# Kernel tuning notes

Measured on AMD Instinct MI355X. Metric: run time of the kernel, lower is better.

## Reference

```python
import jax, jax.numpy as jnp
import numpy as np

PLACEHOLDER = -1
TINY = np.float32(np.finfo(np.float32).tiny)

B, S, V = 128, 8, 32000  # batch, max_spec_len, vocab


def setup_inputs() -> dict:
    key = jax.random.key(0)
    ks = jax.random.split(key, 8)
    # probability tables from softmaxed logits (faithful: rows sum to 1)
    draft_probs = jax.nn.softmax(2.0 * jax.random.normal(ks[0], (B, S, V), dtype=jnp.float32), axis=-1)
    target_probs = jax.nn.softmax(2.0 * jax.random.normal(ks[1], (B, S + 1, V), dtype=jnp.float32), axis=-1)
    draft_token_ids = jax.random.randint(ks[2], (B, S), 0, V, dtype=jnp.int64)
    # variable number of draft tokens per sequence; tail padded with PLACEHOLDER
    lens = jax.random.randint(ks[3], (B,), 1, S + 1)
    draft_token_ids = jnp.where(jnp.arange(S)[None, :] < lens[:, None], draft_token_ids, PLACEHOLDER)
    bonus_token_ids = jax.random.randint(ks[4], (B,), 0, V, dtype=jnp.int64)
    uniform_probs = jax.random.uniform(ks[5], (B, S), dtype=jnp.float32, minval=1e-6, maxval=1.0)
    exp_q = jax.random.exponential(ks[6], (B, V), dtype=jnp.float32)  # q.exponential_()
    is_greedy = jax.random.bernoulli(ks[7], 0.3, (B,))  # temperature == -1 per sequence
    return {
        "draft_token_ids": draft_token_ids,
        "draft_probs": draft_probs,
        "target_probs": target_probs,
        "bonus_token_ids": bonus_token_ids,
        "uniform_probs": uniform_probs,
        "exp_q": exp_q,
        "is_greedy": is_greedy,
    }


def reference(draft_token_ids, draft_probs, target_probs, bonus_token_ids,
              uniform_probs, exp_q, is_greedy):
    b, s = draft_token_ids.shape
    valid = draft_token_ids != PLACEHOLDER                      # [B,S]
    safe_tok = jnp.where(valid, draft_token_ids, 0)

    # gather p_target(tok), p_draft(tok) at each speculative position
    tp = jnp.take_along_axis(target_probs[:, :s], safe_tok[..., None], axis=2)[..., 0]
    dp = jnp.take_along_axis(draft_probs, safe_tok[..., None], axis=2)[..., 0]
    random_accept = (tp / dp) >= uniform_probs                  # [B,S]

    target_argmax = jnp.argmax(target_probs, axis=-1)           # [B,S+1]
    greedy_accept = draft_token_ids == target_argmax[:, :s]

    accept = jnp.where(is_greedy[:, None], greedy_accept, random_accept)

    # recovered token on rejection: argmax of normalized clamp(target - draft) / Exp noise
    adjusted = jnp.clip(target_probs[:, :s] - draft_probs, TINY, None)
    adjusted = adjusted / jnp.sum(adjusted, axis=-1, keepdims=True)
    recovered = jnp.argmax(adjusted / exp_q[:, None, :], axis=-1)  # [B,S]
    replacement = jnp.where(is_greedy[:, None], target_argmax[:, :s], recovered)

    # sequential early-exit scan, vectorized: position p emits iff all earlier
    # positions were valid & accepted and p itself is valid
    step = (valid & accept).astype(jnp.int32)
    alive_prefix = jnp.concatenate(
        [jnp.ones((b, 1), jnp.int32), jnp.cumprod(step, axis=1)[:, :-1]], axis=1).astype(bool)
    emit = valid & alive_prefix                                 # [B,S]

    tokens = jnp.where(accept, draft_token_ids, replacement)
    out = jnp.full((b, s + 1), PLACEHOLDER, dtype=jnp.int64)
    out = out.at[:, :s].set(jnp.where(emit, tokens, PLACEHOLDER))

    num_generated = jnp.sum(emit, axis=1)                       # [B]
    rejected = jnp.any(emit & ~accept, axis=1)                  # [B]
    bonus_val = jnp.where(rejected, PLACEHOLDER, bonus_token_ids)
    out = out.at[jnp.arange(b), num_generated].set(bonus_val)
    return out
```

## Files before the change

### kernel.cpp

```cpp
#include <hip/hip_runtime.h>

#define PLACEHOLDER (-1)
#define TINY_F 1.17549435e-38f
#define MAXS 32
#define SPLIT_G 8
#define SPLIT_R 16

__device__ __forceinline__ void amax_combine(float& bv, int& bi, float v, int i) {
    if (v > bv || (v == bv && i < bi)) { bv = v; bi = i; }
}

__device__ __forceinline__ unsigned long long pack_vi(float v, int i) {
    return ((unsigned long long)__float_as_uint(v) << 32) |
           (unsigned long long)(0xFFFFFFFFu - (unsigned)i);
}

__device__ __forceinline__ int unpack_idx(unsigned long long p) {
    return (int)(0xFFFFFFFFu - (unsigned)(p & 0xFFFFFFFFull));
}

__device__ __forceinline__ void block_argmax(float& bv, int& bi) {
    for (int off = 32; off > 0; off >>= 1) {
        float ov = __shfl_down(bv, off, 64);
        int   oi = __shfl_down(bi, off, 64);
        amax_combine(bv, bi, ov, oi);
    }
    __shared__ float sv[8];
    __shared__ int   si[8];
    int lane = threadIdx.x & 63;
    int w    = threadIdx.x >> 6;
    if (lane == 0) { sv[w] = bv; si[w] = bi; }
    __syncthreads();
    if (threadIdx.x == 0) {
        int nw = (blockDim.x + 63) >> 6;
        for (int k = 1; k < nw; ++k) amax_combine(bv, bi, sv[k], si[k]);
    }
}

__device__ __forceinline__ void wave_argmax_bcast(float& bv, int& bi) {
    for (int off = 32; off > 0; off >>= 1) {
        float ov = __shfl_down(bv, off, 64);
        int   oi = __shfl_down(bi, off, 64);
        amax_combine(bv, bi, ov, oi);
    }
    bv = __shfl(bv, 0, 64);
    bi = __shfl(bi, 0, 64);
}

__global__ void k_main(const float* __restrict__ target_probs,
                       const float* __restrict__ draft_probs,
                       const float* __restrict__ exp_q,
                       const int* __restrict__ draft_ids,
                       const float* __restrict__ uniform,
                       const int* __restrict__ bonus,
                       const int* __restrict__ is_greedy,
                       unsigned long long* __restrict__ ws_g,
                       unsigned long long* __restrict__ ws_r,
                       int* __restrict__ ws_fr,
                       int* __restrict__ out,
                       int B, int S, int V) {
    int total_g = B * SPLIT_G;

    if ((int)blockIdx.x < total_g) {
        int b = blockIdx.x / SPLIT_G;
        int split = blockIdx.x - b * SPLIT_G;
        if (!is_greedy[b]) return;
        if (draft_ids[b * S] == PLACEHOLDER) return;

        int chunk = ((V + SPLIT_G - 1) / SPLIT_G + 3) & ~3;
        int begin = split * chunk;
        int end = begin + chunk; if (end > V) end = V;
        if (begin >= end) return;

        const float* row = target_probs + (size_t)b * (S + 1) * V;
        float bv = 0.0f; int bi = 0x7fffffff;
        int vend = begin + ((end - begin) & ~3);
        const float4* r4 = (const float4*)row;
        for (int j = (begin >> 2) + threadIdx.x; j < (vend >> 2); j += blockDim.x) {
            float4 f = r4[j];
            int base = j << 2;
            amax_combine(bv, bi, f.x, base);
            amax_combine(bv, bi, f.y, base + 1);
            amax_combine(bv, bi, f.z, base + 2);
            amax_combine(bv, bi, f.w, base + 3);
        }
        for (int j = vend + threadIdx.x; j < end; j += blockDim.x)
            amax_combine(bv, bi, row[j], j);
        block_argmax(bv, bi);
        if (threadIdx.x == 0) ws_g[(size_t)b * SPLIT_G + split] = pack_vi(bv, bi);
    } else {
        int t = blockIdx.x - total_g;
        int split = t % SPLIT_R;
        int b = t / SPLIT_R;
        if (is_greedy[b]) return;

        int chunk = ((V + SPLIT_R - 1) / SPLIT_R + 3) & ~3;
        int begin = split * chunk;
        int end = begin + chunk; if (end > V) end = V;
        bool has_work = begin < end;

        const float* erow = exp_q + (size_t)b * V;
        int nj = has_work ? (((end - begin) & ~3) >> 2) : 0;
        const float4* e4 = (const float4*)(erow + begin);
        int tid = threadIdx.x;
        float4 ea = make_float4(0.f, 0.f, 0.f, 0.f), eb = ea;
        if (tid < nj) ea = e4[tid];
        if (tid + (int)blockDim.x < nj) eb = e4[tid + blockDim.x];

        __shared__ int s_tok[MAXS];
        __shared__ unsigned char s_acc[MAXS];
        __shared__ int s_fr;
        if (tid < S) {
            int tok = draft_ids[b * S + tid];
            s_tok[tid] = tok;
            bool acc = false;
            if (tok != PLACEHOLDER) {
                float tp = target_probs[(size_t)b * (S + 1) * V + (size_t)tid * V + tok];
                float dp = draft_probs[(size_t)b * S * V + (size_t)tid * V + tok];
                acc = (tp / dp) >= uniform[b * S + tid];
            }
            s_acc[tid] = acc ? 1 : 0;
        }
        __syncthreads();
        if (tid == 0) {
            int fr = -1;
            for (int q = 0; q < S; ++q) {
                if (s_tok[q] == PLACEHOLDER) break;
                if (!s_acc[q]) { fr = q; break; }
            }
            s_fr = fr;
        }
        __syncthreads();
        int fr = s_fr;

        if (split == 0 && tid == 0) {
            ws_fr[b] = fr;
            int ob = b * (S + 1);
            if (fr < 0) {
                int ng = 0;
                for (int p = 0; p < S; ++p) {
                    if (s_tok[p] == PLACEHOLDER) break;
                    out[ob + p] = s_tok[p];
                    ++ng;
                }
                for (int q = ng; q <= S; ++q) out[ob + q] = PLACEHOLDER;
                out[ob + ng] = bonus[b];
            } else {
                for (int p = 0; p < fr; ++p) out[ob + p] = s_tok[p];
                for (int q = fr; q <= S; ++q) out[ob + q] = PLACEHOLDER;
            }
        }
        if (fr < 0 || !has_work) return;

        const float* trow = target_probs + (size_t)b * (S + 1) * V + (size_t)fr * V;
        const float* drow = draft_probs + (size_t)b * S * V + (size_t)fr * V;
        const float4* t4 = (const float4*)(trow + begin);
        const float4* d4 = (const float4*)(drow + begin);
        float bv = 0.0f; int bi = 0x7fffffff;
        if (tid < nj) {
            float4 tt = t4[tid], dd = d4[tid];
            int base = begin + (tid << 2);
            amax_combine(bv, bi, fmaxf(tt.x - dd.x, TINY_F) / ea.x, base);
            amax_combine(bv, bi, fmaxf(tt.y - dd.y, TINY_F) / ea.y, base + 1);
            amax_combine(bv, bi, fmaxf(tt.z - dd.z, TINY_F) / ea.z, base + 2);
            amax_combine(bv, bi, fmaxf(tt.w - dd.w, TINY_F) / ea.w, base + 3);
        }
        if (tid + (int)blockDim.x < nj) {
            int j = tid + blockDim.x;
            float4 tt = t4[j], dd = d4[j];
            int base = begin + (j << 2);
            amax_combine(bv, bi, fmaxf(tt.x - dd.x, TINY_F) / eb.x, base);
            amax_combine(bv, bi, fmaxf(tt.y - dd.y, TINY_F) / eb.y, base + 1);
            amax_combine(bv, bi, fmaxf(tt.z - dd.z, TINY_F) / eb.z, base + 2);
            amax_combine(bv, bi, fmaxf(tt.w - dd.w, TINY_F) / eb.w, base + 3);
        }
        for (int j = tid + 2 * blockDim.x; j < nj; j += blockDim.x) {
            float4 tt = t4[j], dd = d4[j], ee = e4[j];
            int base = begin + (j << 2);
            amax_combine(bv, bi, fmaxf(tt.x - dd.x, TINY_F) / ee.x, base);
            amax_combine(bv, bi, fmaxf(tt.y - dd.y, TINY_F) / ee.y, base + 1);
            amax_combine(bv, bi, fmaxf(tt.z - dd.z, TINY_F) / ee.z, base + 2);
            amax_combine(bv, bi, fmaxf(tt.w - dd.w, TINY_F) / ee.w, base + 3);
        }
        for (int j = begin + (nj << 2) + tid; j < end; j += blockDim.x)
            amax_combine(bv, bi, fmaxf(trow[j] - drow[j], TINY_F) / erow[j], j);
        block_argmax(bv, bi);
        if (tid == 0) ws_r[(size_t)b * SPLIT_R + split] = pack_vi(bv, bi);
    }
}

__global__ void k_final(const int* __restrict__ draft_ids,
                        const float* __restrict__ target_probs,
                        const int* __restrict__ bonus,
                        const int* __restrict__ is_greedy,
                        const unsigned long long* __restrict__ ws_g,
                        const unsigned long long* __restrict__ ws_r,
                        const int* __restrict__ ws_fr,
                        int* __restrict__ out,
                        int B, int S, int V) {
    int b = blockIdx.x;
    int lane = threadIdx.x;
    int ob = b * (S + 1);

    if (is_greedy[b]) {
        unsigned long long gm = 0ull;
        {
            int chunk = ((V + SPLIT_G - 1) / SPLIT_G + 3) & ~3;
            if (lane < SPLIT_G && lane * chunk < V)
                gm = ws_g[(size_t)b * SPLIT_G + lane];
        }
        for (int off = SPLIT_G / 2; off > 0; off >>= 1) {
            unsigned long long o = __shfl_down(gm, off, 64);
            if (o > gm) gm = o;
        }
        gm = __shfl(gm, 0, 64);
        int am0 = unpack_idx(gm);

        int p = 0, ng = 0;
        bool rej = false;
        while (p < S) {
            int tok = draft_ids[b * S + p];
            if (tok == PLACEHOLDER) break;
            int am;
            if (p == 0) {
                am = am0;
            } else {
                const float* row = target_probs + (size_t)b * (S + 1) * V + (size_t)p * V;
                float bv = 0.0f; int bi = 0x7fffffff;
                int nv4 = V >> 2;
                const float4* r4 = (const float4*)row;
                for (int j = lane; j < nv4; j += 64) {
                    float4 f = r4[j];
                    int base = j << 2;
                    amax_combine(bv, bi, f.x, base);
                    amax_combine(bv, bi, f.y, base + 1);
                    amax_combine(bv, bi, f.z, base + 2);
                    amax_combine(bv, bi, f.w, base + 3);
                }
                for (int j = (nv4 << 2) + lane; j < V; j += 64)
                    amax_combine(bv, bi, row[j], j);
                wave_argmax_bcast(bv, bi);
                am = bi;
            }
            bool acc = (tok == am);
            if (lane == 0) out[ob + p] = acc ? tok : am;
            ++ng;
            if (!acc) { rej = true; break; }
            ++p;
        }
        if (lane == 0) {
            for (int q = ng; q <= S; ++q) out[ob + q] = PLACEHOLDER;
            if (!rej) out[ob + ng] = bonus[b];
        }
    } else {
        int fr = ws_fr[b];
        if (fr < 0) return;
        unsigned long long rm = 0ull;
        {
            int chunk = ((V + SPLIT_R - 1) / SPLIT_R + 3) & ~3;
            if (lane < SPLIT_R && lane * chunk < V)
                rm = ws_r[(size_t)b * SPLIT_R + lane];
        }
        for (int off = SPLIT_R / 2; off > 0; off >>= 1) {
            unsigned long long o = __shfl_down(rm, off, 64);
            if (o > rm) rm = o;
        }
        if (lane == 0) out[ob + fr] = unpack_idx(rm);
    }
}

extern "C" void kernel_launch(void* const* d_in, const int* in_sizes, int n_in,
                              void* d_out, int out_size, void* d_ws, size_t ws_size,
                              hipStream_t stream) {
    const int*   draft_ids    = (const int*)d_in[0];
    const float* draft_probs  = (const float*)d_in[1];
    const float* target_probs = (const float*)d_in[2];
    const int*   bonus        = (const int*)d_in[3];
    const float* uniform      = (const float*)d_in[4];
    const float* exp_q        = (const float*)d_in[5];
    const int*   is_greedy    = (const int*)d_in[6];

    int B = in_sizes[6];
    int S = in_sizes[4] / B;
    int V = in_sizes[5] / B;

    unsigned long long* ws_g = (unsigned long long*)d_ws;
    unsigned long long* ws_r = ws_g + (size_t)B * SPLIT_G;
    int* ws_fr = (int*)(ws_r + (size_t)B * SPLIT_R);
    int* out = (int*)d_out;

    int grid = B * SPLIT_G + B * SPLIT_R;
    k_main<<<grid, 256, 0, stream>>>(target_probs, draft_probs, exp_q, draft_ids,
                                     uniform, bonus, is_greedy,
                                     ws_g, ws_r, ws_fr, out, B, S, V);
    k_final<<<B, 64, 0, stream>>>(draft_ids, target_probs, bonus, is_greedy,
                                  ws_g, ws_r, ws_fr, out, B, S, V);
}
```

Baseline: 15.21 us.

## Double vocab splits, reorder block roles, and early-exit greedy rejection at position zero

Doubles the number of vocabulary splits for both the greedy argmax and the recovered-token argmax, so more blocks share each row. The rejection-sampling blocks now come first in the grid, with the greedy blocks after them. Greedy blocks pre-fill the output row with placeholders, which lets the final kernel return immediately when the first draft token misses the target argmax. That early exit skips the sequential per-position argmax scan in the common rejection case. The trade-off is more blocks and more partial results to combine, plus output writes spread across two kernels.

```diff
diff --git a/kernel.cpp b/kernel.cpp
--- a/kernel.cpp
+++ b/kernel.cpp
@@ -3,8 +3,8 @@
 #define PLACEHOLDER (-1)
 #define TINY_F 1.17549435e-38f
 #define MAXS 32
-#define SPLIT_G 8
-#define SPLIT_R 16
+#define SPLIT_G 16
+#define SPLIT_R 32
 
 __device__ __forceinline__ void amax_combine(float& bv, int& bi, float v, int i) {
     if (v > bv || (v == bv && i < bi)) { bv = v; bi = i; }
@@ -59,39 +59,12 @@
                        int* __restrict__ ws_fr,
                        int* __restrict__ out,
                        int B, int S, int V) {
-    int total_g = B * SPLIT_G;
-
-    if ((int)blockIdx.x < total_g) {
-        int b = blockIdx.x / SPLIT_G;
-        int split = blockIdx.x - b * SPLIT_G;
-        if (!is_greedy[b]) return;
-        if (draft_ids[b * S] == PLACEHOLDER) return;
-
-        int chunk = ((V + SPLIT_G - 1) / SPLIT_G + 3) & ~3;
-        int begin = split * chunk;
-        int end = begin + chunk; if (end > V) end = V;
-        if (begin >= end) return;
-
-        const float* row = target_probs + (size_t)b * (S + 1) * V;
-        float bv = 0.0f; int bi = 0x7fffffff;
-        int vend = begin + ((end - begin) & ~3);
-        const float4* r4 = (const float4*)row;
-        for (int j = (begin >> 2) + threadIdx.x; j < (vend >> 2); j += blockDim.x) {
-            float4 f = r4[j];
-            int base = j << 2;
-            amax_combine(bv, bi, f.x, base);
-            amax_combine(bv, bi, f.y, base + 1);
-            amax_combine(bv, bi, f.z, base + 2);
-            amax_combine(bv, bi, f.w, base + 3);
-        }
-        for (int j = vend + threadIdx.x; j < end; j += blockDim.x)
-            amax_combine(bv, bi, row[j], j);
-        block_argmax(bv, bi);
-        if (threadIdx.x == 0) ws_g[(size_t)b * SPLIT_G + split] = pack_vi(bv, bi);
-    } else {
-        int t = blockIdx.x - total_g;
-        int split = t % SPLIT_R;
-        int b = t / SPLIT_R;
+    int total_r = B * SPLIT_R;
+    int tid = threadIdx.x;
+
+    if ((int)blockIdx.x < total_r) {
+        int b = blockIdx.x / SPLIT_R;
+        int split = blockIdx.x - b * SPLIT_R;
         if (is_greedy[b]) return;
 
         int chunk = ((V + SPLIT_R - 1) / SPLIT_R + 3) & ~3;
@@ -102,7 +75,6 @@
         const float* erow = exp_q + (size_t)b * V;
         int nj = has_work ? (((end - begin) & ~3) >> 2) : 0;
         const float4* e4 = (const float4*)(erow + begin);
-        int tid = threadIdx.x;
         float4 ea = make_float4(0.f, 0.f, 0.f, 0.f), eb = ea;
         if (tid < nj) ea = e4[tid];
         if (tid + (int)blockDim.x < nj) eb = e4[tid + blockDim.x];
@@ -186,6 +158,39 @@
             amax_combine(bv, bi, fmaxf(trow[j] - drow[j], TINY_F) / erow[j], j);
         block_argmax(bv, bi);
         if (tid == 0) ws_r[(size_t)b * SPLIT_R + split] = pack_vi(bv, bi);
+    } else {
+        int t = blockIdx.x - total_r;
+        int b = t / SPLIT_G;
+        int split = t - b * SPLIT_G;
+        if (!is_greedy[b]) return;
+        if (draft_ids[b * S] == PLACEHOLDER) return;
+
+        if (split == 0 && tid == 0) {
+            int ob = b * (S + 1);
+            for (int q = 1; q <= S; ++q) out[ob + q] = PLACEHOLDER;
+        }
+
+        int chunk = ((V + SPLIT_G - 1) / SPLIT_G + 3) & ~3;
+        int begin = split * chunk;
+        int end = begin + chunk; if (end > V) end = V;
+        if (begin >= end) return;
+
+        const float* row = target_probs + (size_t)b * (S + 1) * V;
+        float bv = 0.0f; int bi = 0x7fffffff;
+        int vend = begin + ((end - begin) & ~3);
+        const float4* r4 = (const float4*)row;
+        for (int j = (begin >> 2) + tid; j < (vend >> 2); j += blockDim.x) {
+            float4 f = r4[j];
+            int base = j << 2;
+            amax_combine(bv, bi, f.x, base);
+            amax_combine(bv, bi, f.y, base + 1);
+            amax_combine(bv, bi, f.z, base + 2);
+            amax_combine(bv, bi, f.w, base + 3);
+        }
+        for (int j = vend + tid; j < end; j += blockDim.x)
+            amax_combine(bv, bi, row[j], j);
+        block_argmax(bv, bi);
+        if (tid == 0) ws_g[(size_t)b * SPLIT_G + split] = pack_vi(bv, bi);
     }
 }
 
@@ -215,6 +220,12 @@
         }
         gm = __shfl(gm, 0, 64);
         int am0 = unpack_idx(gm);
+        int tok0 = draft_ids[b * S];
+
+        if (tok0 != am0) {
+            if (lane == 0) out[ob] = am0;
+            return;
+        }
 
         int p = 0, ng = 0;
         bool rej = false;
@@ -289,7 +300,7 @@
     int* ws_fr = (int*)(ws_r + (size_t)B * SPLIT_R);
     int* out = (int*)d_out;
 
-    int grid = B * SPLIT_G + B * SPLIT_R;
+    int grid = B * SPLIT_R + B * SPLIT_G;
     k_main<<<grid, 256, 0, stream>>>(target_probs, draft_probs, exp_q, draft_ids,
                                      uniform, bonus, is_greedy,
                                      ws_g, ws_r, ws_fr, out, B, S, V);
```

Result: slower. 16.71 us (+9.9%).
